# Kernel tuning notes

Measured on AMD Instinct MI355X. Metric: run time of the kernel, lower is better.

## Reference

```python
import jax, jax.numpy as jnp
import numpy as np

B, P, NB, WN, CI, CO = 4, 20000, 9, 17, 64, 128

def setup_inputs() -> dict:
    key = jax.random.key(0)
    k0, k1, k2, k3 = jax.random.split(key, 4)
    in_pc = jax.random.normal(k0, (B, P, CI), dtype=jnp.float32)
    raw_w_weights = jax.random.normal(k1, (P, NB, WN), dtype=jnp.float32) * 0.1
    # padded/missing neighbors use id == P, which indexes the zero-pad row and is masked
    neighbor_ids = jax.random.randint(k2, (P, NB), 0, P + 1)
    weights = jax.random.normal(k3, (WN, CO * CI), dtype=jnp.float32)
    bias = jnp.zeros((P, CO), dtype=jnp.float32)
    return {"in_pc": in_pc, "raw_w_weights": raw_w_weights, "weights": weights,
            "bias": bias, "neighbor_ids": neighbor_ids}

def reference(in_pc, raw_w_weights, weights, bias, neighbor_ids):
    b, p, ci = in_pc.shape
    wn = weights.shape[0]
    co = bias.shape[-1]
    # pc_mask: 1 for real points, 0 for the pad row (id == in_pn)
    nb_mask = (neighbor_ids < p).astype(in_pc.dtype)          # [p, nb]
    w_weights = raw_w_weights * nb_mask[:, :, None]           # [p, nb, wn]
    in_pc_pad = jnp.concatenate(
        [in_pc, jnp.zeros((b, 1, ci), dtype=in_pc.dtype)], axis=1)  # [b, p+1, ci]
    in_neighbors = in_pc_pad[:, neighbor_ids]                 # [b, p, nb, ci] gather
    # weighted fuse over neighbors into wn basis slots
    fuse = jnp.einsum('pnm,bpni->bpmi', w_weights, in_neighbors)   # [b, p, wn, ci]
    Wm = weights.reshape(wn, co, ci)
    # per-basis conv then sum-reduce over wn (b_max_pool=False), fused into one einsum
    out_pc = jnp.einsum('moi,bpmi->bpo', Wm, fuse) + bias      # [b, p, co]
    # is_final_layer=False -> ELU; residual_rate=0 -> no residual branch
    return jax.nn.elu(out_pc)
```

## Files before the change

### kernel.cpp

```cpp
#include <hip/hip_runtime.h>
#include <hip/hip_bf16.h>
#include <stdint.h>

#define B_   4
#define P_   20000
#define NB_  9
#define WN_  17
#define CI_  64
#define CO_  128
#define PTS  16
#define ROWS 64

typedef short bf16x8  __attribute__((ext_vector_type(8)));
typedef float f32x16  __attribute__((ext_vector_type(16)));

union U128 { uint4 u; ushort s[8]; };

__device__ __forceinline__ ushort f2bf(float f) {
    union { float f; uint32_t u; } c; c.f = f;
    uint32_t u = c.u;
    uint32_t r = u + 0x7fff + ((u >> 16) & 1);
    return (ushort)(r >> 16);
}

__global__ __launch_bounds__(256, 2)
void lasm_fused(const float* __restrict__ in_pc,
                const float* __restrict__ raw_w,
                const float* __restrict__ weights,
                const float* __restrict__ bias,
                const int*   __restrict__ nbr,
                float*       __restrict__ out)
{
    __shared__ __align__(16) int    s_nid[PTS][NB_];
    __shared__ __align__(16) float  s_w[PTS][WN_][12];
    __shared__ __align__(16) ushort s_a[ROWS * 64];
    __shared__ __align__(16) ushort s_b[CO_ * 64];

    const int tid  = threadIdx.x;
    const int lane = tid & 63;
    const int wv   = tid >> 6;
    const int p0   = blockIdx.x * PTS;

    if (tid < PTS * NB_) {
        int pl = tid / NB_, n = tid % NB_;
        s_nid[pl][n] = nbr[(p0 + pl) * NB_ + n];
    }
    for (int idx = tid; idx < PTS * NB_ * WN_; idx += 256) {
        int pl = idx / (NB_ * WN_);
        int r  = idx % (NB_ * WN_);
        int n  = r / WN_;
        int m  = r % WN_;
        s_w[pl][m][n] = raw_w[(size_t)(p0 + pl) * NB_ * WN_ + n * WN_ + m];
    }
    for (int idx = tid; idx < PTS * WN_; idx += 256) {
        int pl = idx / WN_, m = idx % WN_;
        s_w[pl][m][9] = 0.f; s_w[pl][m][10] = 0.f; s_w[pl][m][11] = 0.f;
    }
    __syncthreads();

    const int oct = tid & 7;
    const int rp  = tid >> 3;
    float x[2][NB_][8];
    #pragma unroll
    for (int rr = 0; rr < 2; ++rr) {
        int r  = rp + rr * 32;
        int b  = r >> 4;
        int pl = r & 15;
        #pragma unroll
        for (int n = 0; n < NB_; ++n) {
            int nid = s_nid[pl][n];
            if (nid < P_) {
                const float* src = in_pc + ((size_t)(b * P_ + nid)) * CI_ + oct * 8;
                float4 v0 = *(const float4*)(src);
                float4 v1 = *(const float4*)(src + 4);
                x[rr][n][0] = v0.x; x[rr][n][1] = v0.y; x[rr][n][2] = v0.z; x[rr][n][3] = v0.w;
                x[rr][n][4] = v1.x; x[rr][n][5] = v1.y; x[rr][n][6] = v1.z; x[rr][n][7] = v1.w;
            } else {
                #pragma unroll
                for (int j = 0; j < 8; ++j) x[rr][n][j] = 0.f;
            }
        }
    }

    f32x16 acc0, acc1;
    #pragma unroll
    for (int j = 0; j < 16; ++j) { acc0[j] = 0.f; acc1[j] = 0.f; }

    const int co_base = wv * 32;
    const int arow    = lane & 31;
    const int q       = lane >> 5;

    for (int m = 0; m < WN_; ++m) {
        #pragma unroll
        for (int j = 0; j < 4; ++j) {
            int flat = j * 256 + tid;
            int co = flat >> 3, o = flat & 7;
            const float* src = weights + (size_t)m * (CO_ * CI_) + co * CI_ + o * 8;
            float4 v0 = *(const float4*)(src);
            float4 v1 = *(const float4*)(src + 4);
            U128 v;
            v.s[0] = f2bf(v0.x); v.s[1] = f2bf(v0.y); v.s[2] = f2bf(v0.z); v.s[3] = f2bf(v0.w);
            v.s[4] = f2bf(v1.x); v.s[5] = f2bf(v1.y); v.s[6] = f2bf(v1.z); v.s[7] = f2bf(v1.w);
            int op = o ^ (co & 7);
            *(uint4*)&s_b[co * 64 + op * 8] = v.u;
        }
        {
            int pl = rp & 15;
            const float* wrow = &s_w[pl][m][0];
            float4 w0 = *(const float4*)(wrow);
            float4 w1 = *(const float4*)(wrow + 4);
            float  w8 = wrow[8];
            #pragma unroll
            for (int rr = 0; rr < 2; ++rr) {
                int r = rp + rr * 32;
                float c[8];
                #pragma unroll
                for (int j = 0; j < 8; ++j) {
                    c[j] = w0.x * x[rr][0][j] + w0.y * x[rr][1][j]
                         + w0.z * x[rr][2][j] + w0.w * x[rr][3][j]
                         + w1.x * x[rr][4][j] + w1.y * x[rr][5][j]
                         + w1.z * x[rr][6][j] + w1.w * x[rr][7][j]
                         + w8   * x[rr][8][j];
                }
                U128 v;
                #pragma unroll
                for (int j = 0; j < 8; ++j) v.s[j] = f2bf(c[j]);
                int op = oct ^ (r & 7);
                *(uint4*)&s_a[r * 64 + op * 8] = v.u;
            }
        }
        __syncthreads();
        #pragma unroll
        for (int ks = 0; ks < 4; ++ks) {
            int o = ks * 2 + q;
            int bco = co_base + arow;
            bf16x8 bf = *(const bf16x8*)&s_b[bco * 64 + (o ^ (bco & 7)) * 8];
            bf16x8 a0 = *(const bf16x8*)&s_a[arow * 64 + (o ^ (arow & 7)) * 8];
            bf16x8 a1 = *(const bf16x8*)&s_a[(arow + 32) * 64 + (o ^ (arow & 7)) * 8];
            acc0 = __builtin_amdgcn_mfma_f32_32x32x16_bf16(a0, bf, acc0, 0, 0, 0);
            acc1 = __builtin_amdgcn_mfma_f32_32x32x16_bf16(a1, bf, acc1, 0, 0, 0);
        }
        __syncthreads();
    }

    const int col   = co_base + (lane & 31);
    const int rbase = 4 * (lane >> 5);
    #pragma unroll
    for (int mt = 0; mt < 2; ++mt) {
        f32x16 acc = mt ? acc1 : acc0;
        #pragma unroll
        for (int v = 0; v < 16; ++v) {
            int row = mt * 32 + (v & 3) + 8 * (v >> 2) + rbase;
            int b   = row >> 4;
            int p   = p0 + (row & 15);
            float val = acc[v] + bias[(size_t)p * CO_ + col];
            val = (val > 0.f) ? val : (__expf(val) - 1.f);
            out[((size_t)b * P_ + p) * CO_ + col] = val;
        }
    }
}

extern "C" void kernel_launch(void* const* d_in, const int* in_sizes, int n_in,
                              void* d_out, int out_size, void* d_ws, size_t ws_size,
                              hipStream_t stream) {
    const float* in_pc   = (const float*)d_in[0];
    const float* raw_w   = (const float*)d_in[1];
    const float* weights = (const float*)d_in[2];
    const float* bias    = (const float*)d_in[3];
    const int*   nbr     = (const int*)  d_in[4];
    float* out = (float*)d_out;

    lasm_fused<<<dim3(P_ / PTS), dim3(256), 0, stream>>>(
        in_pc, raw_w, weights, bias, nbr, out);
}
```

Baseline: 175.5 us.

## Use fp16 packed math, pre-converted weights, and double-buffered LDS staging

The kernel switches from bf16 to fp16. Neighbor features and fuse weights are stored as packed half2, so the neighbor-fuse step runs as packed fp16 FMAs, and the MFMA becomes the f16 variant. When workspace is available, a small pre-kernel converts and swizzles the weight matrix to fp16 once, so each block copies it instead of converting fp32 to bf16 per block. LDS A/B tiles are double-buffered so the next basis slot is staged while the current MFMAs run, which drops one barrier per iteration. The cost is fp16 accumulation in the neighbor fuse, with possible precision and range risk, plus an extra kernel launch and doubled LDS use.

Result: faster. 169.6 us (-3.4%).

```diff
diff --git a/kernel.cpp b/kernel.cpp
--- a/kernel.cpp
+++ b/kernel.cpp
@@ -11,30 +11,44 @@
 #define PTS  16
 #define ROWS 64
 
-typedef short bf16x8  __attribute__((ext_vector_type(8)));
-typedef float f32x16  __attribute__((ext_vector_type(16)));
-
-union U128 { uint4 u; ushort s[8]; };
-
-__device__ __forceinline__ ushort f2bf(float f) {
-    union { float f; uint32_t u; } c; c.f = f;
-    uint32_t u = c.u;
-    uint32_t r = u + 0x7fff + ((u >> 16) & 1);
-    return (ushort)(r >> 16);
+typedef __fp16 f16x8 __attribute__((ext_vector_type(8)));
+typedef __fp16 h2    __attribute__((ext_vector_type(2)));
+typedef float  f32x16 __attribute__((ext_vector_type(16)));
+
+union H2U { h2 h; uint32_t u; };
+union H8U { __fp16 h[8]; uint4 u; };
+
+__global__ void prep_wm(const float* __restrict__ w, ushort* __restrict__ wsb) {
+    int i = blockIdx.x * 256 + threadIdx.x;
+    int m  = i >> 10;
+    int r  = i & 1023;
+    int co = r >> 3;
+    int o  = r & 7;
+    const float* src = w + (size_t)m * (CO_ * CI_) + co * CI_ + o * 8;
+    float4 v0 = *(const float4*)(src);
+    float4 v1 = *(const float4*)(src + 4);
+    H8U h;
+    *(h2*)&h.h[0] = __builtin_amdgcn_cvt_pkrtz(v0.x, v0.y);
+    *(h2*)&h.h[2] = __builtin_amdgcn_cvt_pkrtz(v0.z, v0.w);
+    *(h2*)&h.h[4] = __builtin_amdgcn_cvt_pkrtz(v1.x, v1.y);
+    *(h2*)&h.h[6] = __builtin_amdgcn_cvt_pkrtz(v1.z, v1.w);
+    *(uint4*)&wsb[m * 8192 + co * 64 + (o ^ (co & 7)) * 8] = h.u;
 }
 
+template <bool PRE>
 __global__ __launch_bounds__(256, 2)
 void lasm_fused(const float* __restrict__ in_pc,
                 const float* __restrict__ raw_w,
                 const float* __restrict__ weights,
                 const float* __restrict__ bias,
                 const int*   __restrict__ nbr,
+                const ushort* __restrict__ wsb,
                 float*       __restrict__ out)
 {
-    __shared__ __align__(16) int    s_nid[PTS][NB_];
-    __shared__ __align__(16) float  s_w[PTS][WN_][12];
-    __shared__ __align__(16) ushort s_a[ROWS * 64];
-    __shared__ __align__(16) ushort s_b[CO_ * 64];
+    __shared__ __align__(16) int      s_nid[PTS][NB_];
+    __shared__ __align__(16) uint32_t s_w2[PTS][WN_][12];
+    __shared__ __align__(16) ushort   s_a[2][ROWS * 64];
+    __shared__ __align__(16) ushort   s_b[2][CO_ * 64];
 
     const int tid  = threadIdx.x;
     const int lane = tid & 63;
@@ -50,17 +64,19 @@
         int r  = idx % (NB_ * WN_);
         int n  = r / WN_;
         int m  = r % WN_;
-        s_w[pl][m][n] = raw_w[(size_t)(p0 + pl) * NB_ * WN_ + n * WN_ + m];
+        float wf = raw_w[(size_t)(p0 + pl) * NB_ * WN_ + n * WN_ + m];
+        H2U c; c.h = __builtin_amdgcn_cvt_pkrtz(wf, wf);
+        s_w2[pl][m][n] = c.u;
     }
     for (int idx = tid; idx < PTS * WN_; idx += 256) {
         int pl = idx / WN_, m = idx % WN_;
-        s_w[pl][m][9] = 0.f; s_w[pl][m][10] = 0.f; s_w[pl][m][11] = 0.f;
+        s_w2[pl][m][9] = 0u; s_w2[pl][m][10] = 0u; s_w2[pl][m][11] = 0u;
     }
     __syncthreads();
 
     const int oct = tid & 7;
     const int rp  = tid >> 3;
-    float x[2][NB_][8];
+    h2 x[2][NB_][4];
     #pragma unroll
     for (int rr = 0; rr < 2; ++rr) {
         int r  = rp + rr * 32;
@@ -73,11 +89,13 @@
                 const float* src = in_pc + ((size_t)(b * P_ + nid)) * CI_ + oct * 8;
                 float4 v0 = *(const float4*)(src);
                 float4 v1 = *(const float4*)(src + 4);
-                x[rr][n][0] = v0.x; x[rr][n][1] = v0.y; x[rr][n][2] = v0.z; x[rr][n][3] = v0.w;
-                x[rr][n][4] = v1.x; x[rr][n][5] = v1.y; x[rr][n][6] = v1.z; x[rr][n][7] = v1.w;
+                x[rr][n][0] = __builtin_amdgcn_cvt_pkrtz(v0.x, v0.y);
+                x[rr][n][1] = __builtin_amdgcn_cvt_pkrtz(v0.z, v0.w);
+                x[rr][n][2] = __builtin_amdgcn_cvt_pkrtz(v1.x, v1.y);
+                x[rr][n][3] = __builtin_amdgcn_cvt_pkrtz(v1.z, v1.w);
             } else {
-                #pragma unroll
-                for (int j = 0; j < 8; ++j) x[rr][n][j] = 0.f;
+                h2 z = {(__fp16)0.f, (__fp16)0.f};
+                x[rr][n][0] = z; x[rr][n][1] = z; x[rr][n][2] = z; x[rr][n][3] = z;
             }
         }
     }
@@ -89,58 +107,84 @@
     const int co_base = wv * 32;
     const int arow    = lane & 31;
     const int q       = lane >> 5;
-
+    const int pl      = rp & 15;
+
+    auto stage_b = [&](int m, int buf) {
+        if (PRE) {
+            #pragma unroll
+            for (int j = 0; j < 4; ++j) {
+                int flat = j * 256 + tid;
+                uint4 v = *(const uint4*)&wsb[m * 8192 + flat * 8];
+                *(uint4*)&s_b[buf][flat * 8] = v;
+            }
+        } else {
+            #pragma unroll
+            for (int j = 0; j < 4; ++j) {
+                int flat = j * 256 + tid;
+                int co = flat >> 3, o = flat & 7;
+                const float* src = weights + (size_t)m * (CO_ * CI_) + co * CI_ + o * 8;
+                float4 v0 = *(const float4*)(src);
+                float4 v1 = *(const float4*)(src + 4);
+                H8U h;
+                *(h2*)&h.h[0] = __builtin_amdgcn_cvt_pkrtz(v0.x, v0.y);
+                *(h2*)&h.h[2] = __builtin_amdgcn_cvt_pkrtz(v0.z, v0.w);
+                *(h2*)&h.h[4] = __builtin_amdgcn_cvt_pkrtz(v1.x, v1.y);
+                *(h2*)&h.h[6] = __builtin_amdgcn_cvt_pkrtz(v1.z, v1.w);
+                *(uint4*)&s_b[buf][co * 64 + (o ^ (co & 7)) * 8] = h.u;
+            }
+        }
+    };
+    auto stage_a = [&](int m, int buf) {
+        const uint32_t* wrow = &s_w2[pl][m][0];
+        uint4 wa = *(const uint4*)(wrow);
+        uint4 wb = *(const uint4*)(wrow + 4);
+        uint32_t w8u = wrow[8];
+        H2U w[9];
+        w[0].u = wa.x; w[1].u = wa.y; w[2].u = wa.z; w[3].u = wa.w;
+        w[4].u = wb.x; w[5].u = wb.y; w[6].u = wb.z; w[7].u = wb.w;
+        w[8].u = w8u;
+        #pragma unroll
+        for (int rr = 0; rr < 2; ++rr) {
+            int r = rp + rr * 32;
+            h2 c0 = {(__fp16)0.f, (__fp16)0.f}, c1 = c0, c2 = c0, c3 = c0;
+            #pragma unroll
+            for (int n = 0; n < NB_; ++n) {
+                h2 wn = w[n].h;
+                c0 += wn * x[rr][n][0];
+                c1 += wn * x[rr][n][1];
+                c2 += wn * x[rr][n][2];
+                c3 += wn * x[rr][n][3];
+            }
+            H8U v;
+            *(h2*)&v.h[0] = c0; *(h2*)&v.h[2] = c1;
+            *(h2*)&v.h[4] = c2; *(h2*)&v.h[6] = c3;
+            *(uint4*)&s_a[buf][r * 64 + (oct ^ (r & 7)) * 8] = v.u;
+        }
+    };
+
+    stage_b(0, 0);
+    stage_a(0, 0);
+    __syncthreads();
+
+    int cur = 0;
     for (int m = 0; m < WN_; ++m) {
-        #pragma unroll
-        for (int j = 0; j < 4; ++j) {
-            int flat = j * 256 + tid;
-            int co = flat >> 3, o = flat & 7;
-            const float* src = weights + (size_t)m * (CO_ * CI_) + co * CI_ + o * 8;
-            float4 v0 = *(const float4*)(src);
-            float4 v1 = *(const float4*)(src + 4);
-            U128 v;
-            v.s[0] = f2bf(v0.x); v.s[1] = f2bf(v0.y); v.s[2] = f2bf(v0.z); v.s[3] = f2bf(v0.w);
-            v.s[4] = f2bf(v1.x); v.s[5] = f2bf(v1.y); v.s[6] = f2bf(v1.z); v.s[7] = f2bf(v1.w);
-            int op = o ^ (co & 7);
-            *(uint4*)&s_b[co * 64 + op * 8] = v.u;
-        }
-        {
-            int pl = rp & 15;
-            const float* wrow = &s_w[pl][m][0];
-            float4 w0 = *(const float4*)(wrow);
-            float4 w1 = *(const float4*)(wrow + 4);
-            float  w8 = wrow[8];
-            #pragma unroll
-            for (int rr = 0; rr < 2; ++rr) {
-                int r = rp + rr * 32;
-                float c[8];
-                #pragma unroll
-                for (int j = 0; j < 8; ++j) {
-                    c[j] = w0.x * x[rr][0][j] + w0.y * x[rr][1][j]
-                         + w0.z * x[rr][2][j] + w0.w * x[rr][3][j]
-                         + w1.x * x[rr][4][j] + w1.y * x[rr][5][j]
-                         + w1.z * x[rr][6][j] + w1.w * x[rr][7][j]
-                         + w8   * x[rr][8][j];
-                }
-                U128 v;
-                #pragma unroll
-                for (int j = 0; j < 8; ++j) v.s[j] = f2bf(c[j]);
-                int op = oct ^ (r & 7);
-                *(uint4*)&s_a[r * 64 + op * 8] = v.u;
-            }
-        }
-        __syncthreads();
+        int nxt = cur ^ 1;
+        if (m + 1 < WN_) {
+            stage_b(m + 1, nxt);
+            stage_a(m + 1, nxt);
+        }
         #pragma unroll
         for (int ks = 0; ks < 4; ++ks) {
             int o = ks * 2 + q;
             int bco = co_base + arow;
-            bf16x8 bf = *(const bf16x8*)&s_b[bco * 64 + (o ^ (bco & 7)) * 8];
-            bf16x8 a0 = *(const bf16x8*)&s_a[arow * 64 + (o ^ (arow & 7)) * 8];
-            bf16x8 a1 = *(const bf16x8*)&s_a[(arow + 32) * 64 + (o ^ (arow & 7)) * 8];
-            acc0 = __builtin_amdgcn_mfma_f32_32x32x16_bf16(a0, bf, acc0, 0, 0, 0);
-            acc1 = __builtin_amdgcn_mfma_f32_32x32x16_bf16(a1, bf, acc1, 0, 0, 0);
+            f16x8 bf = *(const f16x8*)&s_b[cur][bco * 64 + (o ^ (bco & 7)) * 8];
+            f16x8 a0 = *(const f16x8*)&s_a[cur][arow * 64 + (o ^ (arow & 7)) * 8];
+            f16x8 a1 = *(const f16x8*)&s_a[cur][(arow + 32) * 64 + (o ^ (arow & 7)) * 8];
+            acc0 = __builtin_amdgcn_mfma_f32_32x32x16_f16(a0, bf, acc0, 0, 0, 0);
+            acc1 = __builtin_amdgcn_mfma_f32_32x32x16_f16(a1, bf, acc1, 0, 0, 0);
         }
         __syncthreads();
+        cur = nxt;
     }
 
     const int col   = co_base + (lane & 31);
@@ -170,6 +214,14 @@
     const int*   nbr     = (const int*)  d_in[4];
     float* out = (float*)d_out;
 
-    lasm_fused<<<dim3(P_ / PTS), dim3(256), 0, stream>>>(
-        in_pc, raw_w, weights, bias, nbr, out);
+    const size_t need = (size_t)WN_ * CO_ * CI_ * sizeof(ushort);
+    if (d_ws != nullptr && ws_size >= need) {
+        ushort* wsb = (ushort*)d_ws;
+        prep_wm<<<dim3((WN_ * CO_ * 8) / 256), dim3(256), 0, stream>>>(weights, wsb);
+        lasm_fused<true><<<dim3(P_ / PTS), dim3(256), 0, stream>>>(
+            in_pc, raw_w, weights, bias, nbr, wsb, out);
+    } else {
+        lasm_fused<false><<<dim3(P_ / PTS), dim3(256), 0, stream>>>(
+            in_pc, raw_w, weights, bias, nbr, nullptr, out);
+    }
 }
```
